# Performance work log

Measured on AMD Instinct MI355X. Metric: run time of the kernel, lower is better.

The kernel has to match this reference:

```python
import jax, jax.numpy as jnp
import numpy as np

N_E = 1024
E_DIM = 256
N_TOK = 262144


def setup_inputs() -> dict:
    key = jax.random.key(0)
    kx, kw = jax.random.split(key)
    x = jax.random.normal(kx, (N_TOK, E_DIM), dtype=jnp.float32)
    # nn.Embedding weight init: uniform(-1/n_e, 1/n_e)
    emb = jax.random.uniform(kw, (N_E, E_DIM), dtype=jnp.float32,
                             minval=-1.0 / N_E, maxval=1.0 / N_E)
    return {"x": x, "emb": emb}


def reference(x, emb):
    # d[n, k] = ||x_n||^2 + ||e_k||^2 - 2 <x_n, e_k>   -> [N, n_e]
    d = (jnp.sum(x * x, axis=1, keepdims=True)
         + jnp.sum(emb * emb, axis=1)
         - 2.0 * jnp.matmul(x, emb.T))
    min_indices = jnp.argmin(d, axis=1)          # [N] int
    z_q = jnp.take(emb, min_indices, axis=0)     # [N, e_dim]
    return z_q, min_indices
```

## Files before the change

kernel.cpp:

```cpp
#include <hip/hip_runtime.h>


constexpr int N_E   = 1024;
constexpr int E_DIM = 256;
constexpr int N_TOK = 262144;
constexpr float THR = 3e-4f;
constexpr int RGRID  = 1024;
constexpr int RRANGE = N_TOK / RGRID;

typedef __attribute__((ext_vector_type(8))) short short8;
typedef __attribute__((ext_vector_type(4))) float f32x4;

__device__ __forceinline__ float sqf(float v) {
    float p = v * v;
    asm volatile("" : "+v"(p));
    return p;
}
__device__ __forceinline__ float pwb(const float* b, int n) {
    float U[8];
#pragma unroll
    for (int L = 0; L < 8; ++L) {
        float TL  = (sqf(b[L])     + sqf(b[16 + L])) + (sqf(b[32 + L]) + sqf(b[48 + L]));
        float TL8 = (sqf(b[8 + L]) + sqf(b[24 + L])) + (sqf(b[40 + L]) + sqf(b[56 + L]));
        U[L] = TL + TL8;
    }
    float V0 = U[0] + U[4], V1 = U[1] + U[5], V2 = U[2] + U[6], V3 = U[3] + U[7];
    float res = (V0 + V2) + (V1 + V3);
    for (int i = 64; i < n; ++i) res += sqf(b[i]);
    return res;
}
__device__ __forceinline__ float rowsq_exact(const float* r) {
    return sqf(r[0]) + (pwb(r + 1, 120) + (pwb(r + 121, 64) + pwb(r + 185, 71)));
}
__device__ __forceinline__ unsigned short f2bf(float f) {
    union { float f; unsigned u; } v; v.f = f;
    unsigned r = (v.u + 0x7FFF + ((v.u >> 16) & 1)) >> 16;
    return (unsigned short)r;
}

__global__ __launch_bounds__(64) void rowsq_kernel(const float* __restrict__ src,
                                                   float* __restrict__ dst) {
    __shared__ float rs[32][257];
    const int rowBase = blockIdx.x * 32;
    const int tid = threadIdx.x;
    const float4* s4 = reinterpret_cast<const float4*>(src);
    for (int i = tid; i < 32 * 64; i += 64) {
        int rr = i >> 6, c4 = i & 63;
        float4 v = s4[(size_t)(rowBase + rr) * 64 + c4];
        rs[rr][c4 * 4 + 0] = v.x;
        rs[rr][c4 * 4 + 1] = v.y;
        rs[rr][c4 * 4 + 2] = v.z;
        rs[rr][c4 * 4 + 3] = v.w;
    }
    __syncthreads();
    if (tid < 32) dst[rowBase + tid] = rowsq_exact(rs[tid]);
}

__global__ __launch_bounds__(256) void eprep_kernel(const float* __restrict__ emb,
                                                    short8* __restrict__ eb,
                                                    int* __restrict__ cnt) {
    int gid = blockIdx.x * 256 + threadIdx.x;
    if (gid == 0) *cnt = 0;
    int lane = gid & 63;
    int kc   = (gid >> 6) & 7;
    int nt   = gid >> 9;
    int cand = nt * 16 + (lane & 15);
    int k0   = kc * 32 + (lane >> 4) * 8;
    const float4* e4 = reinterpret_cast<const float4*>(emb);
    float4 a = e4[(size_t)cand * 64 + k0 / 4];
    float4 b = e4[(size_t)cand * 64 + k0 / 4 + 1];
    short8 o;
    o[0] = (short)f2bf(a.x); o[1] = (short)f2bf(a.y);
    o[2] = (short)f2bf(a.z); o[3] = (short)f2bf(a.w);
    o[4] = (short)f2bf(b.x); o[5] = (short)f2bf(b.y);
    o[6] = (short)f2bf(b.z); o[7] = (short)f2bf(b.w);
    eb[gid] = o;
}

__global__ __launch_bounds__(256, 4) void score_kernel(const float* __restrict__ x,
                                                       const float* __restrict__ emb,
                                                       const short8* __restrict__ eb,
                                                       const float* __restrict__ B,
                                                       float* __restrict__ zq,
                                                       float* __restrict__ outIdx,
                                                       int* __restrict__ cnt,
                                                       int* __restrict__ list,
                                                       int listCap) {
    __shared__ int fidx[128];
    const int tid = threadIdx.x;
    const int wv  = tid >> 6;
    const int l   = tid & 63;
    const int col = l & 15;
    const int tokW = blockIdx.x * 128 + wv * 32;
    const float4* x4 = reinterpret_cast<const float4*>(x);

    short8 xf[2][8];
#pragma unroll
    for (int mt = 0; mt < 2; ++mt) {
        int row = tokW + mt * 16 + col;
#pragma unroll
        for (int kc = 0; kc < 8; ++kc) {
            const float4* p = x4 + (size_t)row * 64 + kc * 8 + (l >> 4) * 2;
            float4 a = p[0], b = p[1];
            short8 f;
            f[0] = (short)f2bf(a.x); f[1] = (short)f2bf(a.y);
            f[2] = (short)f2bf(a.z); f[3] = (short)f2bf(a.w);
            f[4] = (short)f2bf(b.x); f[5] = (short)f2bf(b.y);
            f[6] = (short)f2bf(b.z); f[7] = (short)f2bf(b.w);
            xf[mt][kc] = f;
        }
    }

    float m1[8], m2[8];
    int   i1[8];
#pragma unroll
    for (int t = 0; t < 8; ++t) { m1[t] = 3.4e38f; m2[t] = 3.4e38f; i1[t] = 0; }

    for (int nt = 0; nt < 64; ++nt) {
        float Bv = B[nt * 16 + col];
        const short8* ep = eb + nt * 512 + l;
        f32x4 acc0 = {0.f, 0.f, 0.f, 0.f}, acc1 = acc0;
#pragma unroll
        for (int kc = 0; kc < 8; ++kc) {
            short8 ef = ep[kc * 64];
            acc0 = __builtin_amdgcn_mfma_f32_16x16x32_bf16(xf[0][kc], ef, acc0, 0, 0, 0);
            acc1 = __builtin_amdgcn_mfma_f32_16x16x32_bf16(xf[1][kc], ef, acc1, 0, 0, 0);
        }
        int idx = nt * 16 + col;
#pragma unroll
        for (int mt = 0; mt < 2; ++mt) {
            f32x4 acc = (mt == 0) ? acc0 : acc1;
#pragma unroll
            for (int r = 0; r < 4; ++r) {
                int t = mt * 4 + r;
                float s = Bv - 2.0f * acc[r];
                bool lt = s < m1[t];
                m2[t] = lt ? m1[t] : fminf(m2[t], s);
                m1[t] = lt ? s : m1[t];
                i1[t] = lt ? idx : i1[t];
            }
        }
    }

#pragma unroll
    for (int off = 1; off <= 8; off <<= 1) {
#pragma unroll
        for (int t = 0; t < 8; ++t) {
            float om1 = __shfl_xor(m1[t], off, 64);
            int   oi  = __shfl_xor(i1[t], off, 64);
            float om2 = __shfl_xor(m2[t], off, 64);
            float nm2 = fminf(fmaxf(m1[t], om1), fminf(m2[t], om2));
            if (om1 < m1[t] || (om1 == m1[t] && oi < i1[t])) { m1[t] = om1; i1[t] = oi; }
            m2[t] = nm2;
        }
    }

    if (col == 0) {
        int g = l >> 4;
#pragma unroll
        for (int mt = 0; mt < 2; ++mt)
#pragma unroll
            for (int r = 0; r < 4; ++r) {
                int t = mt * 4 + r;
                int token = tokW + mt * 16 + g * 4 + r;
                int fl = (m2[t] - m1[t] <= THR) ? 1 : 0;
                outIdx[token] = (float)(i1[t] + (fl ? N_E : 0));
                fidx[wv * 32 + mt * 16 + g * 4 + r] = i1[t];
                if (fl) {
                    int p = atomicAdd(cnt, 1);
                    if (p < listCap) list[p] = token;
                }
            }
    }
    __syncthreads();

    const float4* e4 = reinterpret_cast<const float4*>(emb);
    float4* zq4 = reinterpret_cast<float4*>(zq);
#pragma unroll
    for (int it = 0; it < 32; ++it) {
        int flat = it * 256 + tid;
        int t = flat >> 6, c = flat & 63;
        zq4[((size_t)blockIdx.x * 128 + t) * 64 + c] = e4[(size_t)fidx[t] * 64 + c];
    }
}

__device__ __forceinline__ void process_batch(const float4* x4, const float4* e4,
                                              const float* B, float4* zq4,
                                              float* outIdx,
                                              const int* toks, int m,
                                              float (*xs)[260], float* As,
                                              float (*wmin)[16], int (*widx)[16],
                                              int* bidx, int tid, int wv, int l) {
    for (int i = tid; i < 16 * 64; i += 256) {
        int t = i >> 6, c4 = i & 63;
        float4 v = {0.f, 0.f, 0.f, 0.f};
        if (t < m) v = x4[(size_t)toks[t] * 64 + c4];
        *reinterpret_cast<float4*>(&xs[t][c4 * 4]) = v;
    }
    __syncthreads();
    if (tid < 16) As[tid] = rowsq_exact(xs[tid]);
    __syncthreads();

    const float4* er[4];
#pragma unroll
    for (int j = 0; j < 4; ++j) er[j] = e4 + (size_t)(j * 256 + tid) * 64;

    float acc[16][4];
#pragma unroll
    for (int t = 0; t < 16; ++t)
#pragma unroll
        for (int j = 0; j < 4; ++j) acc[t][j] = 0.f;

    for (int ch = 0; ch < 32; ++ch) {
        float ee[4][8];
#pragma unroll
        for (int j = 0; j < 4; ++j) {
            float4 a = er[j][ch * 2 + 0];
            float4 b = er[j][ch * 2 + 1];
            ee[j][0] = a.x; ee[j][1] = a.y; ee[j][2] = a.z; ee[j][3] = a.w;
            ee[j][4] = b.x; ee[j][5] = b.y; ee[j][6] = b.z; ee[j][7] = b.w;
        }
#pragma unroll
        for (int t = 0; t < 16; ++t) {
            float4 xa = *reinterpret_cast<const float4*>(&xs[t][ch * 8 + 0]);
            float4 xb = *reinterpret_cast<const float4*>(&xs[t][ch * 8 + 4]);
            float xv[8] = {xa.x, xa.y, xa.z, xa.w, xb.x, xb.y, xb.z, xb.w};
#pragma unroll
            for (int j = 0; j < 4; ++j) {
                acc[t][j] += xv[0] * ee[j][0];
                acc[t][j] += xv[1] * ee[j][1];
                acc[t][j] += xv[2] * ee[j][2];
                acc[t][j] += xv[3] * ee[j][3];
                acc[t][j] += xv[4] * ee[j][4];
                acc[t][j] += xv[5] * ee[j][5];
                acc[t][j] += xv[6] * ee[j][6];
                acc[t][j] += xv[7] * ee[j][7];
            }
        }
    }

    float m1[16];
    int   i1[16];
#pragma unroll
    for (int t = 0; t < 16; ++t) { m1[t] = 3.4e38f; i1[t] = 0; }
#pragma unroll
    for (int j = 0; j < 4; ++j) {
        int c = j * 256 + tid;
        float Bc = B[c];
#pragma unroll
        for (int t = 0; t < 16; ++t) {
            float tt = As[t] + Bc;
            float s  = tt - 2.0f * acc[t][j];
            if (s < m1[t]) { m1[t] = s; i1[t] = c; }
        }
    }
#pragma unroll
    for (int off = 1; off <= 32; off <<= 1) {
#pragma unroll
        for (int t = 0; t < 16; ++t) {
            float om = __shfl_xor(m1[t], off, 64);
            int   oi = __shfl_xor(i1[t], off, 64);
            if (om < m1[t] || (om == m1[t] && oi < i1[t])) { m1[t] = om; i1[t] = oi; }
        }
    }
    if (l == 0) {
#pragma unroll
        for (int t = 0; t < 16; ++t) { wmin[wv][t] = m1[t]; widx[wv][t] = i1[t]; }
    }
    __syncthreads();
    if (tid < 16) {
        float bm = wmin[0][tid];
        int   bi = widx[0][tid];
#pragma unroll
        for (int w = 1; w < 4; ++w) {
            float om = wmin[w][tid];
            int   oi = widx[w][tid];
            if (om < bm || (om == bm && oi < bi)) { bm = om; bi = oi; }
        }
        bidx[tid] = bi;
        if (tid < m) outIdx[toks[tid]] = (float)bi;
    }
    __syncthreads();
    for (int i = tid; i < m * 64; i += 256) {
        int t = i >> 6, c4 = i & 63;
        zq4[(size_t)toks[t] * 64 + c4] = e4[(size_t)bidx[t] * 64 + c4];
    }
    __syncthreads();
}

__global__ __launch_bounds__(256) void recheck_kernel(const float* __restrict__ x,
                                                      const float* __restrict__ emb,
                                                      const float* __restrict__ B,
                                                      float* __restrict__ zq,
                                                      float* __restrict__ outIdx,
                                                      const int* __restrict__ cnt,
                                                      const int* __restrict__ list,
                                                      int listCap) {
    __shared__ float xs[16][260];
    __shared__ float As[16];
    __shared__ float wmin[4][16];
    __shared__ int   widx[4][16];
    __shared__ int   bidx[16];
    __shared__ int   lt[RRANGE];
    __shared__ int   kcount;

    const int tid = threadIdx.x;
    const int wv  = tid >> 6;
    const int l   = tid & 63;
    const float4* x4 = reinterpret_cast<const float4*>(x);
    const float4* e4 = reinterpret_cast<const float4*>(emb);
    float4* zq4 = reinterpret_cast<float4*>(zq);

    const int n = *cnt;
    if (n == 0) return;

    if (n <= listCap) {
        const int nsb = (n + 15) >> 4;
        for (int sb = blockIdx.x; sb < nsb; sb += gridDim.x) {
            const int m = (n - sb * 16 < 16) ? (n - sb * 16) : 16;
            if (tid < m) lt[tid] = list[sb * 16 + tid];
            __syncthreads();
            process_batch(x4, e4, B, zq4, outIdx, lt, m,
                          xs, As, wmin, widx, bidx, tid, wv, l);
        }
    } else {
        const int base = blockIdx.x * RRANGE;
        if (tid == 0) kcount = 0;
        __syncthreads();
        for (int i = tid; i < RRANGE; i += 256) {
            float v = outIdx[base + i];
            if (v >= (float)N_E) {
                int p = atomicAdd(&kcount, 1);
                lt[p] = base + i;
            }
        }
        __syncthreads();
        const int k = kcount;
        for (int sb = 0; sb < k; sb += 16) {
            const int m = (k - sb < 16) ? (k - sb) : 16;
            process_batch(x4, e4, B, zq4, outIdx, lt + sb, m,
                          xs, As, wmin, widx, bidx, tid, wv, l);
        }
    }
}

extern "C" void kernel_launch(void* const* d_in, const int* in_sizes, int n_in,
                              void* d_out, int out_size, void* d_ws, size_t ws_size,
                              hipStream_t stream) {
    const float* x   = (const float*)d_in[0];
    const float* emb = (const float*)d_in[1];
    float* out    = (float*)d_out;
    float* zq     = out;
    float* outIdx = out + (size_t)N_TOK * E_DIM;

    char* ws = (char*)d_ws;
    int*    cnt  = (int*)ws;
    float*  B    = (float*)(ws + 4096);
    short8* eb   = (short8*)(ws + 8192);
    int*    list = (int*)(ws + 8192 + 524288);
    long avail = (long)ws_size - (8192 + 524288);
    int listCap = avail > 0 ? (int)(avail / 4) : 0;
    if (listCap > N_TOK) listCap = N_TOK;

    eprep_kernel<<<128, 256, 0, stream>>>(emb, eb, cnt);
    rowsq_kernel<<<N_E / 32, 64, 0, stream>>>(emb, B);
    score_kernel<<<N_TOK / 128, 256, 0, stream>>>(x, emb, eb, B, zq, outIdx, cnt, list, listCap);
    recheck_kernel<<<RGRID, 256, 0, stream>>>(x, emb, B, zq, outIdx, cnt, list, listCap);
}
```

Baseline: 537.4 us.

## Double-buffer codebook fragment loads in score kernel and relax occupancy bound

Rewrites the score loop to process codebook tiles in pairs with two register buffers, so the loads for the next tile are issued before the MFMAs on the current one. This is meant to hide global/L2 load latency behind matrix work. Launch bounds drop from 4 to 2 blocks per SM to make room for the extra 8 short8 registers. The cost is lower occupancy, so there are fewer waves available to hide latency by switching.

```diff
diff --git a/kernel.cpp b/kernel.cpp
--- a/kernel.cpp
+++ b/kernel.cpp
@@ -77,7 +77,25 @@
     eb[gid] = o;
 }
 
-__global__ __launch_bounds__(256, 4) void score_kernel(const float* __restrict__ x,
+__device__ __forceinline__ void top2_update(const f32x4& acc0, const f32x4& acc1,
+                                            float Bv, int idx,
+                                            float* m1, float* m2, int* i1) {
+#pragma unroll
+    for (int mt = 0; mt < 2; ++mt) {
+        const f32x4& acc = mt ? acc1 : acc0;
+#pragma unroll
+        for (int r = 0; r < 4; ++r) {
+            int t = mt * 4 + r;
+            float s = Bv - 2.0f * acc[r];
+            bool lt = s < m1[t];
+            m2[t] = lt ? m1[t] : fminf(m2[t], s);
+            m1[t] = lt ? s : m1[t];
+            i1[t] = lt ? idx : i1[t];
+        }
+    }
+}
+
+__global__ __launch_bounds__(256, 2) void score_kernel(const float* __restrict__ x,
                                                        const float* __restrict__ emb,
                                                        const short8* __restrict__ eb,
                                                        const float* __restrict__ B,
@@ -116,29 +134,38 @@
 #pragma unroll
     for (int t = 0; t < 8; ++t) { m1[t] = 3.4e38f; m2[t] = 3.4e38f; i1[t] = 0; }
 
-    for (int nt = 0; nt < 64; ++nt) {
-        float Bv = B[nt * 16 + col];
-        const short8* ep = eb + nt * 512 + l;
-        f32x4 acc0 = {0.f, 0.f, 0.f, 0.f}, acc1 = acc0;
-#pragma unroll
-        for (int kc = 0; kc < 8; ++kc) {
-            short8 ef = ep[kc * 64];
-            acc0 = __builtin_amdgcn_mfma_f32_16x16x32_bf16(xf[0][kc], ef, acc0, 0, 0, 0);
-            acc1 = __builtin_amdgcn_mfma_f32_16x16x32_bf16(xf[1][kc], ef, acc1, 0, 0, 0);
-        }
-        int idx = nt * 16 + col;
-#pragma unroll
-        for (int mt = 0; mt < 2; ++mt) {
-            f32x4 acc = (mt == 0) ? acc0 : acc1;
-#pragma unroll
-            for (int r = 0; r < 4; ++r) {
-                int t = mt * 4 + r;
-                float s = Bv - 2.0f * acc[r];
-                bool lt = s < m1[t];
-                m2[t] = lt ? m1[t] : fminf(m2[t], s);
-                m1[t] = lt ? s : m1[t];
-                i1[t] = lt ? idx : i1[t];
-            }
+    const short8* ep = eb + l;
+    short8 bufA[8], bufB[8];
+#pragma unroll
+    for (int kc = 0; kc < 8; ++kc) bufA[kc] = ep[kc * 64];
+
+    for (int nt2 = 0; nt2 < 32; ++nt2) {
+        const int nt0 = nt2 * 2;
+#pragma unroll
+        for (int kc = 0; kc < 8; ++kc) bufB[kc] = ep[(nt0 + 1) * 512 + kc * 64];
+        {
+            float Bv = B[nt0 * 16 + col];
+            f32x4 acc0 = {0.f, 0.f, 0.f, 0.f}, acc1 = acc0;
+#pragma unroll
+            for (int kc = 0; kc < 8; ++kc) {
+                acc0 = __builtin_amdgcn_mfma_f32_16x16x32_bf16(xf[0][kc], bufA[kc], acc0, 0, 0, 0);
+                acc1 = __builtin_amdgcn_mfma_f32_16x16x32_bf16(xf[1][kc], bufA[kc], acc1, 0, 0, 0);
+            }
+            top2_update(acc0, acc1, Bv, nt0 * 16 + col, m1, m2, i1);
+        }
+        if (nt2 < 31) {
+#pragma unroll
+            for (int kc = 0; kc < 8; ++kc) bufA[kc] = ep[(nt0 + 2) * 512 + kc * 64];
+        }
+        {
+            float Bv = B[(nt0 + 1) * 16 + col];
+            f32x4 acc0 = {0.f, 0.f, 0.f, 0.f}, acc1 = acc0;
+#pragma unroll
+            for (int kc = 0; kc < 8; ++kc) {
+                acc0 = __builtin_amdgcn_mfma_f32_16x16x32_bf16(xf[0][kc], bufB[kc], acc0, 0, 0, 0);
+                acc1 = __builtin_amdgcn_mfma_f32_16x16x32_bf16(xf[1][kc], bufB[kc], acc1, 0, 0, 0);
+            }
+            top2_update(acc0, acc1, Bv, (nt0 + 1) * 16 + col, m1, m2, i1);
         }
     }
 
```

Result: faster. 487.2 us (-9.3%).

## Stage bf16 codebook tiles through double-buffered LDS with register prefetch

Applied to the files above, without the earlier changes.

Each block cooperatively loads the next 16-entry bf16 codebook tile into registers while the MFMAs for the current tile run, then writes it into the alternate LDS buffer and synchronizes. Previously every wave read its codebook fragments straight from global memory/L2, duplicated across the 4 waves of a block. The goal is to cut redundant global traffic and hide load latency. In exchange it adds a block-wide barrier per tile and 16 KB of LDS, which may limit occupancy at 4 blocks per CU.

```diff
diff --git a/kernel.cpp b/kernel.cpp
--- a/kernel.cpp
+++ b/kernel.cpp
@@ -77,6 +77,24 @@
     eb[gid] = o;
 }
 
+__device__ __forceinline__ void top2_update(const f32x4& acc0, const f32x4& acc1,
+                                            float Bv, int idx,
+                                            float* m1, float* m2, int* i1) {
+#pragma unroll
+    for (int mt = 0; mt < 2; ++mt) {
+        const f32x4& acc = mt ? acc1 : acc0;
+#pragma unroll
+        for (int r = 0; r < 4; ++r) {
+            int t = mt * 4 + r;
+            float s = Bv - 2.0f * acc[r];
+            bool lt = s < m1[t];
+            m2[t] = lt ? m1[t] : fminf(m2[t], s);
+            m1[t] = lt ? s : m1[t];
+            i1[t] = lt ? idx : i1[t];
+        }
+    }
+}
+
 __global__ __launch_bounds__(256, 4) void score_kernel(const float* __restrict__ x,
                                                        const float* __restrict__ emb,
                                                        const short8* __restrict__ eb,
@@ -86,6 +104,7 @@
                                                        int* __restrict__ cnt,
                                                        int* __restrict__ list,
                                                        int listCap) {
+    __shared__ short8 esm[2][512];
     __shared__ int fidx[128];
     const int tid = threadIdx.x;
     const int wv  = tid >> 6;
@@ -116,29 +135,35 @@
 #pragma unroll
     for (int t = 0; t < 8; ++t) { m1[t] = 3.4e38f; m2[t] = 3.4e38f; i1[t] = 0; }
 
+    {
+        short8 r0 = eb[tid];
+        short8 r1 = eb[256 + tid];
+        esm[0][tid]       = r0;
+        esm[0][256 + tid] = r1;
+    }
+    __syncthreads();
+
+    int cur = 0;
     for (int nt = 0; nt < 64; ++nt) {
+        short8 p0, p1;
+        if (nt < 63) {
+            p0 = eb[(nt + 1) * 512 + tid];
+            p1 = eb[(nt + 1) * 512 + 256 + tid];
+        }
         float Bv = B[nt * 16 + col];
-        const short8* ep = eb + nt * 512 + l;
         f32x4 acc0 = {0.f, 0.f, 0.f, 0.f}, acc1 = acc0;
 #pragma unroll
         for (int kc = 0; kc < 8; ++kc) {
-            short8 ef = ep[kc * 64];
+            short8 ef = esm[cur][kc * 64 + l];
             acc0 = __builtin_amdgcn_mfma_f32_16x16x32_bf16(xf[0][kc], ef, acc0, 0, 0, 0);
             acc1 = __builtin_amdgcn_mfma_f32_16x16x32_bf16(xf[1][kc], ef, acc1, 0, 0, 0);
         }
-        int idx = nt * 16 + col;
-#pragma unroll
-        for (int mt = 0; mt < 2; ++mt) {
-            f32x4 acc = (mt == 0) ? acc0 : acc1;
-#pragma unroll
-            for (int r = 0; r < 4; ++r) {
-                int t = mt * 4 + r;
-                float s = Bv - 2.0f * acc[r];
-                bool lt = s < m1[t];
-                m2[t] = lt ? m1[t] : fminf(m2[t], s);
-                m1[t] = lt ? s : m1[t];
-                i1[t] = lt ? idx : i1[t];
-            }
+        top2_update(acc0, acc1, Bv, nt * 16 + col, m1, m2, i1);
+        if (nt < 63) {
+            esm[cur ^ 1][tid]       = p0;
+            esm[cur ^ 1][256 + tid] = p1;
+            __syncthreads();
+            cur ^= 1;
         }
     }
 
```

After: 476.8 us, median of 3. 1.13x faster.

## Stage codebook tiles in double-buffered LDS and software-pipeline MFMA with top-2 update

Applied to the files above, without the earlier changes.

Codebook bf16 tiles are now loaded cooperatively by the whole block into a double-buffered shared-memory array instead of each wave reading them straight from global memory. Two 16-column tiles are processed per step, and the top-2 reduction for the previous pair overlaps with the MFMAs of the current pair while the next pair is prefetched into registers. Each block of four waves now fetches the codebook once rather than four times, and the compare chain is taken off the MFMA critical path. In exchange it adds a barrier per step, 32KB of LDS, more live accumulator registers, and lowers the launch-bounds occupancy hint from 4 to 3 blocks.

```diff
diff --git a/kernel.cpp b/kernel.cpp
--- a/kernel.cpp
+++ b/kernel.cpp
@@ -77,7 +77,74 @@
     eb[gid] = o;
 }
 
-__global__ __launch_bounds__(256, 4) void score_kernel(const float* __restrict__ x,
+__device__ __forceinline__ void top2_pair(const f32x4& a0, const f32x4& a1,
+                                          const f32x4& b0, const f32x4& b1,
+                                          const float* __restrict__ B,
+                                          int pairIdx, int col,
+                                          float* m1, float* m2, int* i1) {
+    float BvA = B[(pairIdx * 2 + 0) * 16 + col];
+    float BvB = B[(pairIdx * 2 + 1) * 16 + col];
+    int idxA = (pairIdx * 2 + 0) * 16 + col;
+    int idxB = (pairIdx * 2 + 1) * 16 + col;
+#pragma unroll
+    for (int mt = 0; mt < 2; ++mt) {
+        const f32x4& accA = mt ? a1 : a0;
+#pragma unroll
+        for (int r = 0; r < 4; ++r) {
+            int t = mt * 4 + r;
+            float s = BvA - 2.0f * accA[r];
+            bool lt = s < m1[t];
+            m2[t] = lt ? m1[t] : fminf(m2[t], s);
+            m1[t] = lt ? s : m1[t];
+            i1[t] = lt ? idxA : i1[t];
+        }
+    }
+#pragma unroll
+    for (int mt = 0; mt < 2; ++mt) {
+        const f32x4& accB = mt ? b1 : b0;
+#pragma unroll
+        for (int r = 0; r < 4; ++r) {
+            int t = mt * 4 + r;
+            float s = BvB - 2.0f * accB[r];
+            bool lt = s < m1[t];
+            m2[t] = lt ? m1[t] : fminf(m2[t], s);
+            m1[t] = lt ? s : m1[t];
+            i1[t] = lt ? idxB : i1[t];
+        }
+    }
+}
+
+#define MFMA_PAIR(A0, A1, B0, B1, bufbase)                                          \
+    {                                                                               \
+        A0 = (f32x4){0.f, 0.f, 0.f, 0.f}; A1 = A0; B0 = A0; B1 = A0;                \
+        _Pragma("unroll")                                                           \
+        for (int kc = 0; kc < 8; ++kc) {                                            \
+            short8 efA = esm[(bufbase) + kc * 64 + l];                              \
+            short8 efB = esm[(bufbase) + 512 + kc * 64 + l];                        \
+            A0 = __builtin_amdgcn_mfma_f32_16x16x32_bf16(xf[0][kc], efA, A0, 0, 0, 0); \
+            A1 = __builtin_amdgcn_mfma_f32_16x16x32_bf16(xf[1][kc], efA, A1, 0, 0, 0); \
+            B0 = __builtin_amdgcn_mfma_f32_16x16x32_bf16(xf[0][kc], efB, B0, 0, 0, 0); \
+            B1 = __builtin_amdgcn_mfma_f32_16x16x32_bf16(xf[1][kc], efB, B1, 0, 0, 0); \
+        }                                                                           \
+    }
+
+#define PREFETCH_PAIR(pp)                                                           \
+    {                                                                               \
+        p0 = eb[(pp) * 1024 + tid];                                                 \
+        p1 = eb[(pp) * 1024 + 256 + tid];                                           \
+        p2 = eb[(pp) * 1024 + 512 + tid];                                           \
+        p3 = eb[(pp) * 1024 + 768 + tid];                                           \
+    }
+
+#define WRITE_PAIR(bufbase)                                                         \
+    {                                                                               \
+        esm[(bufbase) + tid]       = p0;                                            \
+        esm[(bufbase) + 256 + tid] = p1;                                            \
+        esm[(bufbase) + 512 + tid] = p2;                                            \
+        esm[(bufbase) + 768 + tid] = p3;                                            \
+    }
+
+__global__ __launch_bounds__(256, 3) void score_kernel(const float* __restrict__ x,
                                                        const float* __restrict__ emb,
                                                        const short8* __restrict__ eb,
                                                        const float* __restrict__ B,
@@ -86,6 +153,7 @@
                                                        int* __restrict__ cnt,
                                                        int* __restrict__ list,
                                                        int listCap) {
+    __shared__ short8 esm[2048];
     __shared__ int fidx[128];
     const int tid = threadIdx.x;
     const int wv  = tid >> 6;
@@ -116,31 +184,38 @@
 #pragma unroll
     for (int t = 0; t < 8; ++t) { m1[t] = 3.4e38f; m2[t] = 3.4e38f; i1[t] = 0; }
 
-    for (int nt = 0; nt < 64; ++nt) {
-        float Bv = B[nt * 16 + col];
-        const short8* ep = eb + nt * 512 + l;
-        f32x4 acc0 = {0.f, 0.f, 0.f, 0.f}, acc1 = acc0;
-#pragma unroll
-        for (int kc = 0; kc < 8; ++kc) {
-            short8 ef = ep[kc * 64];
-            acc0 = __builtin_amdgcn_mfma_f32_16x16x32_bf16(xf[0][kc], ef, acc0, 0, 0, 0);
-            acc1 = __builtin_amdgcn_mfma_f32_16x16x32_bf16(xf[1][kc], ef, acc1, 0, 0, 0);
-        }
-        int idx = nt * 16 + col;
-#pragma unroll
-        for (int mt = 0; mt < 2; ++mt) {
-            f32x4 acc = (mt == 0) ? acc0 : acc1;
-#pragma unroll
-            for (int r = 0; r < 4; ++r) {
-                int t = mt * 4 + r;
-                float s = Bv - 2.0f * acc[r];
-                bool lt = s < m1[t];
-                m2[t] = lt ? m1[t] : fminf(m2[t], s);
-                m1[t] = lt ? s : m1[t];
-                i1[t] = lt ? idx : i1[t];
-            }
-        }
-    }
+    short8 p0, p1, p2, p3;
+    f32x4 aE0, aE1, bE0, bE1;
+    f32x4 aO0, aO1, bO0, bO1;
+
+    PREFETCH_PAIR(0);
+    WRITE_PAIR(0);
+    __syncthreads();
+    int cur = 0;
+
+    PREFETCH_PAIR(1);
+    MFMA_PAIR(aE0, aE1, bE0, bE1, cur * 1024);
+    WRITE_PAIR((cur ^ 1) * 1024);
+    __syncthreads();
+    cur ^= 1;
+
+    for (int p = 1; p < 31; p += 2) {
+        PREFETCH_PAIR(p + 1);
+        MFMA_PAIR(aO0, aO1, bO0, bO1, cur * 1024);
+        top2_pair(aE0, aE1, bE0, bE1, B, p - 1, col, m1, m2, i1);
+        WRITE_PAIR((cur ^ 1) * 1024);
+        __syncthreads();
+        cur ^= 1;
+        PREFETCH_PAIR(p + 2);
+        MFMA_PAIR(aE0, aE1, bE0, bE1, cur * 1024);
+        top2_pair(aO0, aO1, bO0, bO1, B, p, col, m1, m2, i1);
+        WRITE_PAIR((cur ^ 1) * 1024);
+        __syncthreads();
+        cur ^= 1;
+    }
+    MFMA_PAIR(aO0, aO1, bO0, bO1, cur * 1024);
+    top2_pair(aE0, aE1, bE0, bE1, B, 30, col, m1, m2, i1);
+    top2_pair(aO0, aO1, bO0, bO1, B, 31, col, m1, m2, i1);
 
 #pragma unroll
     for (int off = 1; off <= 8; off <<= 1) {
```

After: 502.5 us. 1.07x faster.
